# Kernel optimization log

Measured on AMD Instinct MI355X. Metric: run time of the kernel, lower is better.

Reference implementation:

```python
import jax, jax.numpy as jnp
import numpy as np

EPS = 1e-05


def setup_inputs() -> dict:
    key = jax.random.key(0)
    k0, k1, k2, k3, k4 = jax.random.split(key, 5)
    B, N, D = 8, 4096, 1024
    scale = 1.0 / np.sqrt(D)  # roughly xavier scale for D x D
    return {
        "x": jax.random.normal(k0, (B, N, D), dtype=jnp.float32),
        "w_query_real": jax.random.normal(k1, (D, D), dtype=jnp.float32) * scale,
        "w_query_imag": jax.random.normal(k2, (D, D), dtype=jnp.float32) * scale,
        "w_key": jax.random.normal(k3, (D, D), dtype=jnp.float32) * scale,
        "w_value": jax.random.normal(k4, (D, D), dtype=jnp.float32) * scale,
    }


def reference(x, w_query_real, w_query_imag, w_key, w_value):
    # x is real -> x_real = x_imag = x (torch fallback branch)
    q_real = jnp.einsum('bnd,de->bne', x, w_query_real)
    q_imag = jnp.einsum('bnd,de->bne', x, w_query_imag)
    query = jax.nn.relu(q_real) * jax.nn.relu(q_imag)  # relu gating; dropout p=0

    key = jnp.einsum('bnd,de->bne', x, w_key)
    value = jnp.einsum('bnd,de->bne', x, w_value)
    # L2 norm over the sequence axis (dim=1), keepdim
    key = key / (jnp.linalg.norm(key, axis=1, keepdims=True) + EPS)
    value = value / (jnp.linalg.norm(value, axis=1, keepdims=True) + EPS)

    kv_attn = jax.nn.relu(jnp.einsum('bnd,bne->bde', key, value))  # [B, D, D]
    return jnp.einsum('bnd,bde->bne', query, kv_attn)
```

## Files before the change

kernel.cpp:

```cpp
#include <hip/hip_runtime.h>
#include <stdint.h>
#include <stddef.h>

#define D_ 1024
#define NSEQ_ 4096
#define BATCH_ 8
#define BN_ (BATCH_ * NSEQ_)

typedef __attribute__((ext_vector_type(8))) short short8;
typedef __attribute__((ext_vector_type(4))) short short4_t;
typedef __attribute__((ext_vector_type(4))) float float4_t;

__device__ __forceinline__ short f2b(float f) {
  union { float f; uint32_t u; } x; x.f = f;
  uint32_t r = x.u + 0x7fffu + ((x.u >> 16) & 1u);
  return (short)(r >> 16);
}
__device__ __forceinline__ float b2f(short s) {
  union { float f; uint32_t u; } x; x.u = ((uint32_t)(uint16_t)s) << 16; return x.f;
}

__device__ __forceinline__ void gll16(const void* g, void* l) {
  auto gp = reinterpret_cast<const uint32_t __attribute__((address_space(1)))*>(
      reinterpret_cast<uintptr_t>(g));
  auto lp = reinterpret_cast<uint32_t __attribute__((address_space(3)))*>(
      reinterpret_cast<uintptr_t>(l));
  __builtin_amdgcn_global_load_lds(gp, lp, 16, 0, 0);
}

#define MFMA16(a, b, c) __builtin_amdgcn_mfma_f32_16x16x32_bf16(a, b, c, 0, 0, 0)

__global__ void convert_x(const float* __restrict__ X, short* __restrict__ Xb) {
  const size_t i = (size_t)blockIdx.x * 256 + threadIdx.x;
  const float4_t* p = (const float4_t*)(X + i * 8);
  float4_t a = __builtin_nontemporal_load(p);
  float4_t b = __builtin_nontemporal_load(p + 1);
  short8 o;
  o[0] = f2b(a.x); o[1] = f2b(a.y); o[2] = f2b(a.z); o[3] = f2b(a.w);
  o[4] = f2b(b.x); o[5] = f2b(b.y); o[6] = f2b(b.z); o[7] = f2b(b.w);
  *(short8*)(Xb + i * 8) = o;
}

__global__ void transpose_convert_w(const float* __restrict__ w0, const float* __restrict__ w1,
                                    const float* __restrict__ w2, const float* __restrict__ w3,
                                    short* __restrict__ wT) {
  __shared__ float tile[32][33];
  const int z = blockIdx.z;
  const float* src = (z == 0) ? w0 : (z == 1) ? w1 : (z == 2) ? w2 : w3;
  const int d0 = blockIdx.y * 32, e0 = blockIdx.x * 32;
  const int tx = threadIdx.x, ty = threadIdx.y;
#pragma unroll
  for (int i = 0; i < 4; ++i) {
    int d = ty + i * 8;
    tile[d][tx] = __builtin_nontemporal_load(&src[(size_t)(d0 + d) * D_ + (e0 + tx)]);
  }
  __syncthreads();
#pragma unroll
  for (int i = 0; i < 4; ++i) {
    int e = ty + i * 8;
    const int eg = e0 + e;
    const int row = ((eg >> 4) << 6) + (z << 4) + (eg & 15);
    wT[(size_t)row * D_ + (d0 + tx)] = f2b(tile[tx][e]);
  }
}

__global__ __launch_bounds__(512, 2) void gemm_x4w(
    const short* __restrict__ Xb, const short* __restrict__ Wint,
    short* __restrict__ qout, short* __restrict__ kT, short* __restrict__ vT,
    float* __restrict__ ssk, float* __restrict__ ssv) {
  __shared__ short ring[4 * 16384];

  const int t = threadIdx.x;
  const int w = t >> 6;
  const int lane = t & 63;
  const int l16 = lane & 15;
  const int quad = lane >> 4;
  const int wm = w >> 2;
  const int wn = w & 3;

  const int bid = blockIdx.x;
  const int lin = (bid & 7) * 256 + (bid >> 3);
  const int mt = lin >> 4;
  const int nt = lin & 15;
  const int M0 = mt * 256;
  const int N0 = nt * 256;
  const int E0 = nt * 64;

  const float4_t fz = {0.f, 0.f, 0.f, 0.f};
  float4_t acc[8][4];
#pragma unroll
  for (int i = 0; i < 8; ++i)
#pragma unroll
    for (int j2 = 0; j2 < 4; ++j2) acc[i][j2] = fz;

  size_t goffA[2], goffB[2];
  int ldsu[2];
#pragma unroll
  for (int r = 0; r < 2; ++r) {
    const int uu = w * 2 + r;
    const int row = uu * 16 + (lane >> 2);
    const int sp = (lane & 3) ^ ((row >> 1) & 3);
    goffA[r] = (size_t)(M0 + row) * 1024 + sp * 8;
    goffB[r] = (size_t)(N0 + row) * 1024 + sp * 8;
    ldsu[r] = uu * 512;
  }
  int aoff[8], boff[4];
#pragma unroll
  for (int i = 0; i < 8; ++i) {
    const int row = wm * 128 + i * 16 + l16;
    aoff[i] = row * 32 + ((quad ^ ((row >> 1) & 3)) << 3);
  }
#pragma unroll
  for (int j2 = 0; j2 < 4; ++j2) {
    const int row = wn * 64 + j2 * 16 + l16;
    boff[j2] = row * 32 + ((quad ^ ((row >> 1) & 3)) << 3);
  }

#pragma unroll
  for (int s = 0; s < 3; ++s) {
#pragma unroll
    for (int r = 0; r < 2; ++r) gll16(Xb + goffA[r] + s * 32, ring + s * 16384 + ldsu[r]);
#pragma unroll
    for (int r = 0; r < 2; ++r) gll16(Wint + goffB[r] + s * 32, ring + s * 16384 + 8192 + ldsu[r]);
  }
  asm volatile("s_waitcnt vmcnt(8)" ::: "memory");
  __builtin_amdgcn_s_barrier();

#pragma unroll 1
  for (int tt = 0; tt < 32; ++tt) {
    const short* As = ring + (tt & 3) * 16384;
    const short* Bs = As + 8192;
    short8 aF[8], bF[4];

#pragma unroll
    for (int i = 0; i < 4; ++i) aF[i] = *(const short8*)&As[aoff[i]];
#pragma unroll
    for (int j2 = 0; j2 < 4; ++j2) bF[j2] = *(const short8*)&Bs[boff[j2]];
    if (tt < 29) {
      short* dA = ring + ((tt + 3) & 3) * 16384;
      const int k0 = (tt + 3) * 32;
#pragma unroll
      for (int r = 0; r < 2; ++r) gll16(Xb + goffA[r] + k0, dA + ldsu[r]);
    }
    __builtin_amdgcn_s_barrier();
    asm volatile("s_waitcnt lgkmcnt(0)" ::: "memory");
    __builtin_amdgcn_s_setprio(1);
#pragma unroll
    for (int i = 0; i < 4; ++i)
#pragma unroll
      for (int j2 = 0; j2 < 4; ++j2) acc[i][j2] = MFMA16(aF[i], bF[j2], acc[i][j2]);
    __builtin_amdgcn_s_setprio(0);
    __builtin_amdgcn_s_barrier();

#pragma unroll
    for (int i = 4; i < 8; ++i) aF[i] = *(const short8*)&As[aoff[i]];
    if (tt < 29) {
      short* dB = ring + ((tt + 3) & 3) * 16384 + 8192;
      const int k0 = (tt + 3) * 32;
#pragma unroll
      for (int r = 0; r < 2; ++r) gll16(Wint + goffB[r] + k0, dB + ldsu[r]);
    }
    __builtin_amdgcn_s_barrier();
    asm volatile("s_waitcnt lgkmcnt(0)" ::: "memory");
    __builtin_amdgcn_s_setprio(1);
#pragma unroll
    for (int i = 4; i < 8; ++i)
#pragma unroll
      for (int j2 = 0; j2 < 4; ++j2) acc[i][j2] = MFMA16(aF[i], bF[j2], acc[i][j2]);
    __builtin_amdgcn_s_setprio(0);
    if (tt < 29) {
      asm volatile("s_waitcnt vmcnt(8)" ::: "memory");
    } else if (tt == 29) {
      asm volatile("s_waitcnt vmcnt(4)" ::: "memory");
    } else if (tt == 30) {
      asm volatile("s_waitcnt vmcnt(0)" ::: "memory");
    }
    __builtin_amdgcn_s_barrier();
  }

  const int e = E0 + wn * 16 + l16;
#pragma unroll
  for (int i = 0; i < 8; ++i) {
    const int rowg = M0 + wm * 128 + i * 16 + quad * 4;
#pragma unroll
    for (int rr = 0; rr < 4; ++rr) {
      float v = fmaxf(acc[i][0][rr], 0.f) * fmaxf(acc[i][1][rr], 0.f);
      qout[(size_t)(rowg + rr) * 1024 + e] = f2b(v);
    }
  }

  short* T = ring;
  const int b = M0 >> 12;
  const int n0 = M0 & 4095;
#pragma unroll
  for (int wt = 2; wt < 4; ++wt) {
    short* dst = (wt == 2) ? kT : vT;
    float* ss = (wt == 2) ? ssk : ssv;
    __syncthreads();
#pragma unroll
    for (int i = 0; i < 8; ++i) {
      const int nl = wm * 128 + i * 16 + quad * 4;
      const int el = wn * 16 + l16;
      short4_t pk;
#pragma unroll
      for (int rr = 0; rr < 4; ++rr) pk[rr] = f2b(acc[i][wt][rr]);
      *(short4_t*)&T[el * 264 + nl] = pk;
    }
    __syncthreads();
#pragma unroll
    for (int it = 0; it < 4; ++it) {
      const int ee = it * 16 + (t >> 5);
      const int nch = (t & 31) * 8;
      short8 vv = *(const short8*)&T[ee * 264 + nch];
      *(short8*)&dst[((size_t)b * 1024 + E0 + ee) * 4096 + n0 + nch] = vv;
      float s = 0.f;
#pragma unroll
      for (int x2 = 0; x2 < 8; ++x2) { float f = b2f(vv[x2]); s += f * f; }
      s += __shfl_xor(s, 1, 32);
      s += __shfl_xor(s, 2, 32);
      s += __shfl_xor(s, 4, 32);
      s += __shfl_xor(s, 8, 32);
      s += __shfl_xor(s, 16, 32);
      if ((t & 31) == 0) atomicAdd(&ss[b * 1024 + E0 + ee], s);
    }
  }
}

__global__ void finish_norms(const float* __restrict__ ss, float* __restrict__ inv) {
  const int i = blockIdx.x * 256 + threadIdx.x;
  if (i < 2 * BATCH_ * D_) inv[i] = 1.f / (sqrtf(ss[i]) + 1e-5f);
}

__global__ __launch_bounds__(512, 2) void gemm_bt_p(
    const short* __restrict__ A, const short* __restrict__ Bm,
    size_t sAb, size_t sBb, int K, int mode,
    const float* __restrict__ rsb, const float* __restrict__ csb,
    void* __restrict__ outp) {
  __shared__ short ring[4 * 12288];

  const int t = threadIdx.x;
  const int w = t >> 6;
  const int lane = t & 63;
  const int l16 = lane & 15;
  const int quad = lane >> 4;
  const int wm = w >> 2;
  const int wn = w & 3;
  const int M0 = blockIdx.y * 128, N0 = blockIdx.x * 256, b = blockIdx.z;
  const short* Ab = A + (size_t)b * sAb;
  const short* Bb = Bm + (size_t)b * sBb;
  const int NT = K >> 5;

  const float4_t fz = {0.f, 0.f, 0.f, 0.f};
  float4_t acc[4][4];
#pragma unroll
  for (int i = 0; i < 4; ++i)
#pragma unroll
    for (int j = 0; j < 4; ++j) acc[i][j] = fz;

  const short* gptr[3];
  int ldso[3];
#pragma unroll
  for (int r = 0; r < 3; ++r) {
    const int u = w * 3 + r;
    const int lrow = (u < 8 ? u * 16 : (u - 8) * 16) + (lane >> 2);
    const int sp = (lane & 3) ^ ((lrow >> 1) & 3);
    gptr[r] = (u < 8 ? Ab + (size_t)(M0 + lrow) * K : Bb + (size_t)(N0 + lrow) * K) + sp * 8;
    ldso[r] = (u < 8 ? u * 512 : 4096 + (u - 8) * 512);
  }
  int aoff[4], boff[4];
#pragma unroll
  for (int i = 0; i < 4; ++i) {
    const int row = wm * 64 + i * 16 + l16;
    aoff[i] = row * 32 + ((quad ^ ((row >> 1) & 3)) << 3);
  }
#pragma unroll
  for (int j = 0; j < 4; ++j) {
    const int row = wn * 64 + j * 16 + l16;
    boff[j] = 4096 + row * 32 + ((quad ^ ((row >> 1) & 3)) << 3);
  }

#pragma unroll
  for (int s = 0; s < 3; ++s)
#pragma unroll
    for (int r = 0; r < 3; ++r) gll16(gptr[r] + s * 32, ring + s * 12288 + ldso[r]);
  asm volatile("s_waitcnt vmcnt(6)" ::: "memory");
  __builtin_amdgcn_s_barrier();

#pragma unroll 1
  for (int tt = 0; tt < NT; ++tt) {
    const short* As = ring + (tt & 3) * 12288;
    short8 aF[4], bF[4];
#pragma unroll
    for (int i = 0; i < 4; ++i) aF[i] = *(const short8*)&As[aoff[i]];
#pragma unroll
    for (int j = 0; j < 4; ++j) bF[j] = *(const short8*)&As[boff[j]];
    if (tt < NT - 3) {
      short* dS = ring + ((tt + 3) & 3) * 12288;
      const int k0 = (tt + 3) * 32;
#pragma unroll
      for (int r = 0; r < 3; ++r) gll16(gptr[r] + k0, dS + ldso[r]);
    }
    __builtin_amdgcn_s_barrier();
    asm volatile("s_waitcnt lgkmcnt(0)" ::: "memory");
    __builtin_amdgcn_s_setprio(1);
#pragma unroll
    for (int i = 0; i < 4; ++i)
#pragma unroll
      for (int j = 0; j < 4; ++j) acc[i][j] = MFMA16(aF[i], bF[j], acc[i][j]);
    __builtin_amdgcn_s_setprio(0);
    if (tt < NT - 3) {
      asm volatile("s_waitcnt vmcnt(6)" ::: "memory");
    } else if (tt == NT - 3) {
      asm volatile("s_waitcnt vmcnt(3)" ::: "memory");
    } else if (tt == NT - 2) {
      asm volatile("s_waitcnt vmcnt(0)" ::: "memory");
    }
    __builtin_amdgcn_s_barrier();
  }

  if (mode == 0) {
    short* ob = (short*)outp + (size_t)b * D_ * D_;
    const float* rs = rsb + b * D_ + M0;
    const float* cs = csb + b * D_ + N0;
#pragma unroll
    for (int i = 0; i < 4; ++i) {
      const int rl = wm * 64 + i * 16 + quad * 4;
#pragma unroll
      for (int j = 0; j < 4; ++j) {
        const int cl = wn * 64 + j * 16 + l16;
        const float csc = cs[cl];
#pragma unroll
        for (int rr = 0; rr < 4; ++rr) {
          float v = acc[i][j][rr] * rs[rl + rr] * csc;
          v = fmaxf(v, 0.f);
          ob[(size_t)(M0 + rl + rr) * 1024 + (N0 + cl)] = f2b(v);
        }
      }
    }
  } else {
    float* of = (float*)outp + (size_t)b * NSEQ_ * D_;
#pragma unroll
    for (int i = 0; i < 4; ++i) {
      const int rl = wm * 64 + i * 16 + quad * 4;
#pragma unroll
      for (int j = 0; j < 4; ++j) {
        const int cl = wn * 64 + j * 16 + l16;
#pragma unroll
        for (int rr = 0; rr < 4; ++rr)
          __builtin_nontemporal_store(acc[i][j][rr],
                                      &of[(size_t)(M0 + rl + rr) * 1024 + (N0 + cl)]);
      }
    }
  }
}

extern "C" void kernel_launch(void* const* d_in, const int* in_sizes, int n_in,
                              void* d_out, int out_size, void* d_ws, size_t ws_size,
                              hipStream_t stream) {
  const float* x = (const float*)d_in[0];
  const float* wqr = (const float*)d_in[1];
  const float* wqi = (const float*)d_in[2];
  const float* wk = (const float*)d_in[3];
  const float* wv = (const float*)d_in[4];

  short* wT = (short*)d_ws;
  short* qb = wT + (size_t)4 * D_ * D_;
  short* kT = qb + (size_t)BN_ * D_;
  short* vT = kT + (size_t)BATCH_ * D_ * NSEQ_;
  short* kvT = vT + (size_t)BATCH_ * D_ * NSEQ_;
  float* ssk = (float*)(kvT + (size_t)BATCH_ * D_ * D_);
  float* ssv = ssk + BATCH_ * D_;
  float* invk = ssv + BATCH_ * D_;
  float* invv = invk + BATCH_ * D_;

  short* xb = (short*)d_out;

  hipMemsetAsync(ssk, 0, (size_t)2 * BATCH_ * D_ * sizeof(float), stream);

  convert_x<<<dim3(16384), 256, 0, stream>>>(x, xb);

  transpose_convert_w<<<dim3(32, 32, 4), dim3(32, 8), 0, stream>>>(wqr, wqi, wk, wv, wT);

  gemm_x4w<<<dim3(2048), 512, 0, stream>>>(xb, wT, qb, kT, vT, ssk, ssv);

  finish_norms<<<dim3(64), 256, 0, stream>>>(ssk, invk);

  gemm_bt_p<<<dim3(4, 8, 8), 512, 0, stream>>>(
      vT, kT, (size_t)D_ * NSEQ_, (size_t)D_ * NSEQ_, 4096, 0, invv, invk, (void*)kvT);

  gemm_bt_p<<<dim3(4, 32, 8), 512, 0, stream>>>(
      qb, kvT, (size_t)NSEQ_ * D_, (size_t)D_ * D_, 1024, 1, nullptr, nullptr, d_out);
}
```

Baseline: 687.6 us.

## Double-buffer MFMA fragments in registers to overlap LDS reads with compute

Both GEMM main loops are restructured so the next k-tile's A/B fragments are read from LDS into a second register set while the current set feeds the MFMAs. The loop is unrolled by two with ping-pong register arrays, and there is now one barrier per step instead of two or three. The vmcnt wait thresholds are adjusted to match the new issue order. This is meant to hide LDS latency and cut barrier stalls, at the cost of more VGPRs (which may hurt occupancy at launch_bounds 512,2). NT must be even for the unrolled loop to be correct.

After: 674.3 us. About the same (-1.9%).

```diff
diff --git a/kernel.cpp b/kernel.cpp
--- a/kernel.cpp
+++ b/kernel.cpp
@@ -64,6 +64,37 @@
   }
 }
 
+#define X4W_STEP(TT, AC, BC, AN, BN2)                                          \
+  {                                                                            \
+    const int tt_ = (TT);                                                      \
+    if (tt_ < 30) { asm volatile("s_waitcnt vmcnt(4)" ::: "memory"); }         \
+    else if (tt_ == 30) { asm volatile("s_waitcnt vmcnt(0)" ::: "memory"); }   \
+    if (tt_ < 31) __builtin_amdgcn_s_barrier();                                \
+    if (tt_ < 31) {                                                            \
+      const short* Asn = ring + ((tt_ + 1) & 3) * 16384;                       \
+      const short* Bsn = Asn + 8192;                                           \
+      _Pragma("unroll")                                                        \
+      for (int i_ = 0; i_ < 8; ++i_) AN[i_] = *(const short8*)&Asn[aoff[i_]];  \
+      _Pragma("unroll")                                                        \
+      for (int j_ = 0; j_ < 4; ++j_) BN2[j_] = *(const short8*)&Bsn[boff[j_]]; \
+    }                                                                          \
+    if (tt_ <= 28) {                                                           \
+      short* dS = ring + ((tt_ + 3) & 3) * 16384;                              \
+      const int k0_ = (tt_ + 3) * 32;                                          \
+      _Pragma("unroll")                                                        \
+      for (int r_ = 0; r_ < 2; ++r_) gll16(Xb + goffA[r_] + k0_, dS + ldsu[r_]); \
+      _Pragma("unroll")                                                        \
+      for (int r_ = 0; r_ < 2; ++r_) gll16(Wint + goffB[r_] + k0_, dS + 8192 + ldsu[r_]); \
+    }                                                                          \
+    __builtin_amdgcn_s_setprio(1);                                             \
+    _Pragma("unroll")                                                          \
+    for (int i_ = 0; i_ < 8; ++i_)                                             \
+      _Pragma("unroll")                                                        \
+      for (int j_ = 0; j_ < 4; ++j_)                                           \
+        acc[i_][j_] = MFMA16(AC[i_], BC[j_], acc[i_][j_]);                     \
+    __builtin_amdgcn_s_setprio(0);                                             \
+  }
+
 __global__ __launch_bounds__(512, 2) void gemm_x4w(
     const short* __restrict__ Xb, const short* __restrict__ Wint,
     short* __restrict__ qout, short* __restrict__ kT, short* __restrict__ vT,
@@ -123,59 +154,19 @@
 #pragma unroll
     for (int r = 0; r < 2; ++r) gll16(Wint + goffB[r] + s * 32, ring + s * 16384 + 8192 + ldsu[r]);
   }
-  asm volatile("s_waitcnt vmcnt(8)" ::: "memory");
+  asm volatile("s_waitcnt vmcnt(4)" ::: "memory");
   __builtin_amdgcn_s_barrier();
 
+  short8 aFA[8], bFA[4], aFB[8], bFB[4];
+#pragma unroll
+  for (int i = 0; i < 8; ++i) aFA[i] = *(const short8*)&ring[aoff[i]];
+#pragma unroll
+  for (int j2 = 0; j2 < 4; ++j2) bFA[j2] = *(const short8*)&ring[8192 + boff[j2]];
+
 #pragma unroll 1
-  for (int tt = 0; tt < 32; ++tt) {
-    const short* As = ring + (tt & 3) * 16384;
-    const short* Bs = As + 8192;
-    short8 aF[8], bF[4];
-
-#pragma unroll
-    for (int i = 0; i < 4; ++i) aF[i] = *(const short8*)&As[aoff[i]];
-#pragma unroll
-    for (int j2 = 0; j2 < 4; ++j2) bF[j2] = *(const short8*)&Bs[boff[j2]];
-    if (tt < 29) {
-      short* dA = ring + ((tt + 3) & 3) * 16384;
-      const int k0 = (tt + 3) * 32;
-#pragma unroll
-      for (int r = 0; r < 2; ++r) gll16(Xb + goffA[r] + k0, dA + ldsu[r]);
-    }
-    __builtin_amdgcn_s_barrier();
-    asm volatile("s_waitcnt lgkmcnt(0)" ::: "memory");
-    __builtin_amdgcn_s_setprio(1);
-#pragma unroll
-    for (int i = 0; i < 4; ++i)
-#pragma unroll
-      for (int j2 = 0; j2 < 4; ++j2) acc[i][j2] = MFMA16(aF[i], bF[j2], acc[i][j2]);
-    __builtin_amdgcn_s_setprio(0);
-    __builtin_amdgcn_s_barrier();
-
-#pragma unroll
-    for (int i = 4; i < 8; ++i) aF[i] = *(const short8*)&As[aoff[i]];
-    if (tt < 29) {
-      short* dB = ring + ((tt + 3) & 3) * 16384 + 8192;
-      const int k0 = (tt + 3) * 32;
-#pragma unroll
-      for (int r = 0; r < 2; ++r) gll16(Wint + goffB[r] + k0, dB + ldsu[r]);
-    }
-    __builtin_amdgcn_s_barrier();
-    asm volatile("s_waitcnt lgkmcnt(0)" ::: "memory");
-    __builtin_amdgcn_s_setprio(1);
-#pragma unroll
-    for (int i = 4; i < 8; ++i)
-#pragma unroll
-      for (int j2 = 0; j2 < 4; ++j2) acc[i][j2] = MFMA16(aF[i], bF[j2], acc[i][j2]);
-    __builtin_amdgcn_s_setprio(0);
-    if (tt < 29) {
-      asm volatile("s_waitcnt vmcnt(8)" ::: "memory");
-    } else if (tt == 29) {
-      asm volatile("s_waitcnt vmcnt(4)" ::: "memory");
-    } else if (tt == 30) {
-      asm volatile("s_waitcnt vmcnt(0)" ::: "memory");
-    }
-    __builtin_amdgcn_s_barrier();
+  for (int tt = 0; tt < 32; tt += 2) {
+    X4W_STEP(tt, aFA, bFA, aFB, bFB);
+    X4W_STEP(tt + 1, aFB, bFB, aFA, bFA);
   }
 
   const int e = E0 + wn * 16 + l16;
@@ -230,6 +221,34 @@
   const int i = blockIdx.x * 256 + threadIdx.x;
   if (i < 2 * BATCH_ * D_) inv[i] = 1.f / (sqrtf(ss[i]) + 1e-5f);
 }
+
+#define BTP_STEP(TT, AC, BC, AN, BN2)                                          \
+  {                                                                            \
+    const int tt_ = (TT);                                                      \
+    if (tt_ < NT - 2) { asm volatile("s_waitcnt vmcnt(3)" ::: "memory"); }     \
+    else if (tt_ == NT - 2) { asm volatile("s_waitcnt vmcnt(0)" ::: "memory"); } \
+    if (tt_ < NT - 1) __builtin_amdgcn_s_barrier();                            \
+    if (tt_ < NT - 1) {                                                        \
+      const short* Sn = ring + ((tt_ + 1) & 3) * 12288;                        \
+      _Pragma("unroll")                                                        \
+      for (int i_ = 0; i_ < 4; ++i_) AN[i_] = *(const short8*)&Sn[aoff[i_]];   \
+      _Pragma("unroll")                                                        \
+      for (int j_ = 0; j_ < 4; ++j_) BN2[j_] = *(const short8*)&Sn[boff[j_]];  \
+    }                                                                          \
+    if (tt_ <= NT - 4) {                                                       \
+      short* dS = ring + ((tt_ + 3) & 3) * 12288;                              \
+      const int k0_ = (tt_ + 3) * 32;                                          \
+      _Pragma("unroll")                                                        \
+      for (int r_ = 0; r_ < 3; ++r_) gll16(gptr[r_] + k0_, dS + ldso[r_]);     \
+    }                                                                          \
+    __builtin_amdgcn_s_setprio(1);                                             \
+    _Pragma("unroll")                                                          \
+    for (int i_ = 0; i_ < 4; ++i_)                                             \
+      _Pragma("unroll")                                                        \
+      for (int j_ = 0; j_ < 4; ++j_)                                           \
+        acc[i_][j_] = MFMA16(AC[i_], BC[j_], acc[i_][j_]);                     \
+    __builtin_amdgcn_s_setprio(0);                                             \
+  }
 
 __global__ __launch_bounds__(512, 2) void gemm_bt_p(
     const short* __restrict__ A, const short* __restrict__ Bm,
@@ -283,39 +302,19 @@
   for (int s = 0; s < 3; ++s)
 #pragma unroll
     for (int r = 0; r < 3; ++r) gll16(gptr[r] + s * 32, ring + s * 12288 + ldso[r]);
-  asm volatile("s_waitcnt vmcnt(6)" ::: "memory");
+  asm volatile("s_waitcnt vmcnt(3)" ::: "memory");
   __builtin_amdgcn_s_barrier();
 
+  short8 aFA[4], bFA[4], aFB[4], bFB[4];
+#pragma unroll
+  for (int i = 0; i < 4; ++i) aFA[i] = *(const short8*)&ring[aoff[i]];
+#pragma unroll
+  for (int j = 0; j < 4; ++j) bFA[j] = *(const short8*)&ring[boff[j]];
+
 #pragma unroll 1
-  for (int tt = 0; tt < NT; ++tt) {
-    const short* As = ring + (tt & 3) * 12288;
-    short8 aF[4], bF[4];
-#pragma unroll
-    for (int i = 0; i < 4; ++i) aF[i] = *(const short8*)&As[aoff[i]];
-#pragma unroll
-    for (int j = 0; j < 4; ++j) bF[j] = *(const short8*)&As[boff[j]];
-    if (tt < NT - 3) {
-      short* dS = ring + ((tt + 3) & 3) * 12288;
-      const int k0 = (tt + 3) * 32;
-#pragma unroll
-      for (int r = 0; r < 3; ++r) gll16(gptr[r] + k0, dS + ldso[r]);
-    }
-    __builtin_amdgcn_s_barrier();
-    asm volatile("s_waitcnt lgkmcnt(0)" ::: "memory");
-    __builtin_amdgcn_s_setprio(1);
-#pragma unroll
-    for (int i = 0; i < 4; ++i)
-#pragma unroll
-      for (int j = 0; j < 4; ++j) acc[i][j] = MFMA16(aF[i], bF[j], acc[i][j]);
-    __builtin_amdgcn_s_setprio(0);
-    if (tt < NT - 3) {
-      asm volatile("s_waitcnt vmcnt(6)" ::: "memory");
-    } else if (tt == NT - 3) {
-      asm volatile("s_waitcnt vmcnt(3)" ::: "memory");
-    } else if (tt == NT - 2) {
-      asm volatile("s_waitcnt vmcnt(0)" ::: "memory");
-    }
-    __builtin_amdgcn_s_barrier();
+  for (int tt = 0; tt < NT; tt += 2) {
+    BTP_STEP(tt, aFA, bFA, aFB, bFB);
+    BTP_STEP(tt + 1, aFB, bFB, aFA, bFA);
   }
 
   if (mode == 0) {
```
